# Performance work log

Measured on AMD Instinct MI355X. Metric: run time of the kernel, lower is better.

Reference implementation:

```python
import jax, jax.numpy as jnp
import numpy as np

REG_MAX = 16
NUM_CLASSES = 80
STRIDES = (8, 16, 32)
FEAT_SIZES = ((80, 80), (40, 40), (20, 20))
CLS_DIM = 256
REG_DIM = 256
B = 16


def setup_inputs() -> dict:
    key = jax.random.key(0)
    ks = jax.random.split(key, 32)
    inp = {}
    i = 0
    for l, (H, W) in enumerate(FEAT_SIZES):
        inp[f"cls_feat{l}"] = jax.random.normal(ks[i], (B, CLS_DIM, H, W), jnp.float32); i += 1
        inp[f"reg_feat{l}"] = jax.random.normal(ks[i], (B, REG_DIM, H, W), jnp.float32); i += 1
    bias_init = -float(np.log((1.0 - 0.01) / 0.01))
    for l in range(3):
        inp[f"obj_w{l}"] = jax.random.normal(ks[i], (1, REG_DIM), jnp.float32) * 0.02; i += 1
        inp[f"obj_b{l}"] = jnp.full((1,), bias_init, jnp.float32)
        inp[f"cls_w{l}"] = jax.random.normal(ks[i], (NUM_CLASSES, CLS_DIM), jnp.float32) * 0.02; i += 1
        inp[f"cls_b{l}"] = jnp.full((NUM_CLASSES,), bias_init, jnp.float32)
        inp[f"reg_w{l}"] = jax.random.normal(ks[i], (4 * REG_MAX, REG_DIM), jnp.float32) * 0.02; i += 1
        inp[f"reg_b{l}"] = jnp.ones((4 * REG_MAX,), jnp.float32)
    return inp


def _anchors(H, W, stride):
    ay, ax = jnp.meshgrid(jnp.arange(H, dtype=jnp.float32), jnp.arange(W, dtype=jnp.float32), indexing="ij")
    a = jnp.stack([ax, ay], axis=-1).reshape(-1, 2)  # [HW, 2] (x, y)
    return (a + 0.5) * stride


def _level(cls_feat, reg_feat, obj_w, obj_b, cls_w, cls_b, reg_w, reg_b, stride):
    Bb, _, H, W = cls_feat.shape
    M = H * W
    # 1x1 convs as channel contractions; output in [B, H, W, O] then flatten to [B, M, O]
    obj = (jnp.einsum("bchw,oc->bhwo", reg_feat, obj_w) + obj_b).reshape(Bb, M, 1)
    cls = (jnp.einsum("bchw,oc->bhwo", cls_feat, cls_w) + cls_b).reshape(Bb, M, NUM_CLASSES)
    reg = (jnp.einsum("bchw,oc->bhwo", reg_feat, reg_w) + reg_b).reshape(Bb, M, 4 * REG_MAX)
    # DFL decode: softmax over bins, expectation with proj = linspace(0, reg_max, reg_max)
    proj = jnp.linspace(0.0, float(REG_MAX), REG_MAX)
    dist = jax.nn.softmax(reg.reshape(Bb, M, 4, REG_MAX), axis=-1)
    reg_d = jnp.einsum("bmfr,r->bmf", dist, proj)  # [B, M, 4] (l, t, r, b)
    anchors = _anchors(H, W, stride)  # [M, 2]
    x1y1 = anchors[None] - reg_d[..., :2] * stride
    x2y2 = anchors[None] + reg_d[..., 2:] * stride
    box = jnp.concatenate([x1y1, x2y2], axis=-1)  # [B, M, 4]
    return jnp.concatenate([obj, cls, reg, box], axis=-1)  # [B, M, 1+80+64+4]


def reference(cls_feat0, cls_feat1, cls_feat2, reg_feat0, reg_feat1, reg_feat2,
              obj_w0, obj_b0, cls_w0, cls_b0, reg_w0, reg_b0,
              obj_w1, obj_b1, cls_w1, cls_b1, reg_w1, reg_b1,
              obj_w2, obj_b2, cls_w2, cls_b2, reg_w2, reg_b2):
    lvl0 = _level(cls_feat0, reg_feat0, obj_w0, obj_b0, cls_w0, cls_b0, reg_w0, reg_b0, STRIDES[0])
    lvl1 = _level(cls_feat1, reg_feat1, obj_w1, obj_b1, cls_w1, cls_b1, reg_w1, reg_b1, STRIDES[1])
    lvl2 = _level(cls_feat2, reg_feat2, obj_w2, obj_b2, cls_w2, cls_b2, reg_w2, reg_b2, STRIDES[2])
    # concat anchors along M: [B, 8400, 149]
    return jnp.concatenate([lvl0, lvl1, lvl2], axis=1)
```

## Files before the change

kernel.cpp:

```cpp
#include <hip/hip_runtime.h>
#include <stdint.h>

typedef __attribute__((ext_vector_type(4))) float f32x4;
typedef __attribute__((ext_vector_type(8))) short s16x8;

struct Params {
  const float* cls_feat[3];
  const float* reg_feat[3];
  const float* obj_w[3];
  const float* obj_b[3];
  const float* cls_w[3];
  const float* cls_b[3];
  const float* reg_w[3];
  const float* reg_b[3];
  float* out;
};

__device__ __forceinline__ unsigned short f2bf(float f) {
  unsigned int u = __builtin_bit_cast(unsigned int, f);
  u = (u + 0x7FFFu + ((u >> 16) & 1u)) >> 16;
  return (unsigned short)u;
}

#define LDS_PITCH 264

__global__ __launch_bounds__(320) void head_kernel(Params p) {
  const int tid  = threadIdx.x;
  const int lane = tid & 63;
  const int wave = tid >> 6;
  const int quad = lane >> 4;
  const int col  = lane & 15;
  const bool is_cls = (blockIdx.y == 0);

  int bx = blockIdx.x;
  int b  = bx / 132;
  int t  = bx - b * 132;
  int level, tloc;
  if (t < 100)      { level = 0; tloc = t; }
  else if (t < 125) { level = 1; tloc = t - 100; }
  else              { level = 2; tloc = t - 125; }

  const int   LW_[3]   = {80, 40, 20};
  const int   LM_[3]   = {6400, 1600, 400};
  const float LS_[3]   = {8.f, 16.f, 32.f};
  const int   LOFF_[3] = {0, 6400, 8000};

  const int   Mlvl = LM_[level];
  const int   Moff = LOFF_[level];
  const float strd = LS_[level];
  const int   m0   = tloc * 64;
  int valid = Mlvl - m0; if (valid > 64) valid = 64;

  __shared__ __align__(16) short lds_feat[64 * LDS_PITCH];
  __shared__ float g_lds[4][64];

  const float* featp = (is_cls ? p.cls_feat[level] : p.reg_feat[level])
                       + (size_t)b * 256 * (size_t)Mlvl;
  {
    const int mloc = tid & 63;
    int mg = m0 + mloc; if (mg > Mlvl - 1) mg = Mlvl - 1;
    const float* colp = featp + mg;
    for (int cb = wave; cb < 32; cb += 5) {
      const int c0 = cb * 8;
      float f[8];
      #pragma unroll
      for (int j = 0; j < 8; ++j) f[j] = colp[(size_t)(c0 + j) * Mlvl];
      s16x8 h;
      #pragma unroll
      for (int j = 0; j < 8; ++j) h[j] = (short)f2bf(f[j]);
      *(s16x8*)&lds_feat[mloc * LDS_PITCH + c0] = h;
    }
  }

  s16x8 afrag[8];
  {
    const int orow = wave * 16 + col;
    const float* wptr = nullptr;
    if (is_cls) {
      wptr = p.cls_w[level] + orow * 256;
    } else {
      if (orow < 64)       wptr = p.reg_w[level] + orow * 256;
      else if (orow == 64) wptr = p.obj_w[level];
    }
    #pragma unroll
    for (int s = 0; s < 8; ++s) {
      s16x8 a = {0, 0, 0, 0, 0, 0, 0, 0};
      if (wptr) {
        const f32x4* wp = (const f32x4*)(wptr + s * 32 + quad * 8);
        f32x4 w0 = wp[0], w1 = wp[1];
        a[0] = (short)f2bf(w0[0]); a[1] = (short)f2bf(w0[1]);
        a[2] = (short)f2bf(w0[2]); a[3] = (short)f2bf(w0[3]);
        a[4] = (short)f2bf(w1[0]); a[5] = (short)f2bf(w1[1]);
        a[6] = (short)f2bf(w1[2]); a[7] = (short)f2bf(w1[3]);
      }
      afrag[s] = a;
    }
  }

  float bias[4];
  #pragma unroll
  for (int r = 0; r < 4; ++r) {
    const int o = wave * 16 + quad * 4 + r;
    if (is_cls) bias[r] = p.cls_b[level][o];
    else        bias[r] = (o < 64) ? p.reg_b[level][o]
                        : ((o == 64) ? p.obj_b[level][0] : 0.f);
  }

  __syncthreads();

  f32x4 acc[4];
  #pragma unroll
  for (int mf = 0; mf < 4; ++mf) {
    f32x4 d = {0.f, 0.f, 0.f, 0.f};
    const short* brow = &lds_feat[(mf * 16 + col) * LDS_PITCH + quad * 8];
    #pragma unroll
    for (int s = 0; s < 8; ++s) {
      s16x8 bfrag = *(const s16x8*)(brow + s * 32);
      d = __builtin_amdgcn_mfma_f32_16x16x32_bf16(afrag[s], bfrag, d, 0, 0, 0);
    }
    acc[mf] = d;
  }

  const size_t outbase = (size_t)b * 8400 + Moff + m0;
  float* out = p.out;

  if (is_cls) {
    #pragma unroll
    for (int mf = 0; mf < 4; ++mf) {
      const int m = mf * 16 + col;
      if (m < valid) {
        const size_t rowp = (outbase + m) * 149 + 1 + wave * 16 + quad * 4;
        #pragma unroll
        for (int r = 0; r < 4; ++r) out[rowp + r] = acc[mf][r] + bias[r];
      }
    }
  } else if (wave < 4) {
    const float projscale = 16.f / 15.f;
    #pragma unroll
    for (int mf = 0; mf < 4; ++mf) {
      const int m = mf * 16 + col;
      const float v0 = acc[mf][0] + bias[0];
      const float v1 = acc[mf][1] + bias[1];
      const float v2 = acc[mf][2] + bias[2];
      const float v3 = acc[mf][3] + bias[3];
      if (m < valid) {
        const size_t rowp = (outbase + m) * 149 + 81 + wave * 16 + quad * 4;
        out[rowp + 0] = v0; out[rowp + 1] = v1;
        out[rowp + 2] = v2; out[rowp + 3] = v3;
      }
      float mx = fmaxf(fmaxf(v0, v1), fmaxf(v2, v3));
      mx = fmaxf(mx, __shfl_xor(mx, 16, 64));
      mx = fmaxf(mx, __shfl_xor(mx, 32, 64));
      const float e0 = __expf(v0 - mx), e1 = __expf(v1 - mx);
      const float e2 = __expf(v2 - mx), e3 = __expf(v3 - mx);
      float s = e0 + e1 + e2 + e3;
      const float q4 = (float)(quad * 4);
      float n = q4 * e0 + (q4 + 1.f) * e1 + (q4 + 2.f) * e2 + (q4 + 3.f) * e3;
      s += __shfl_xor(s, 16, 64); s += __shfl_xor(s, 32, 64);
      n += __shfl_xor(n, 16, 64); n += __shfl_xor(n, 32, 64);
      if (quad == 0) g_lds[wave][m] = projscale * n / s;
    }
  } else {
    #pragma unroll
    for (int mf = 0; mf < 4; ++mf) {
      const int m = mf * 16 + col;
      if (quad == 0 && m < valid)
        out[(outbase + m) * 149] = acc[mf][0] + bias[0];
    }
  }

  __syncthreads();

  if (!is_cls && wave == 4) {
    const int m = lane;
    if (m < valid) {
      const float g0 = g_lds[0][m], g1 = g_lds[1][m];
      const float g2 = g_lds[2][m], g3 = g_lds[3][m];
      const int mg = m0 + m;
      int hh;
      if (level == 0)      hh = mg / 80;
      else if (level == 1) hh = mg / 40;
      else                 hh = mg / 20;
      const int ww = mg - hh * LW_[level];
      const float ax = (ww + 0.5f) * strd;
      const float ay = (hh + 0.5f) * strd;
      const size_t rowp = (outbase + m) * 149 + 145;
      out[rowp + 0] = ax - g0 * strd;
      out[rowp + 1] = ay - g1 * strd;
      out[rowp + 2] = ax + g2 * strd;
      out[rowp + 3] = ay + g3 * strd;
    }
  }
}

extern "C" void kernel_launch(void* const* d_in, const int* in_sizes, int n_in,
                              void* d_out, int out_size, void* d_ws, size_t ws_size,
                              hipStream_t stream) {
  (void)in_sizes; (void)n_in; (void)out_size; (void)d_ws; (void)ws_size;
  Params p;
  p.cls_feat[0] = (const float*)d_in[0];
  p.reg_feat[0] = (const float*)d_in[1];
  p.cls_feat[1] = (const float*)d_in[2];
  p.reg_feat[1] = (const float*)d_in[3];
  p.cls_feat[2] = (const float*)d_in[4];
  p.reg_feat[2] = (const float*)d_in[5];
  for (int l = 0; l < 3; ++l) {
    const int base = 6 + l * 6;
    p.obj_w[l] = (const float*)d_in[base + 0];
    p.obj_b[l] = (const float*)d_in[base + 1];
    p.cls_w[l] = (const float*)d_in[base + 2];
    p.cls_b[l] = (const float*)d_in[base + 3];
    p.reg_w[l] = (const float*)d_in[base + 4];
    p.reg_b[l] = (const float*)d_in[base + 5];
  }
  p.out = (float*)d_out;

  dim3 grid(16 * 132, 2);
  dim3 block(320);
  hipLaunchKernelGGL(head_kernel, grid, block, 0, stream, p);
}
```

Measured before the change: 376.4 us.

## Use 80-anchor tiles with swizzled LDS, prefetched feature loads, vector stores

Tiles now cover 80 anchors instead of 64. Every level divides evenly, so the ragged tail checks go away and the grid shrinks. The padded LDS pitch is replaced by an XOR swizzle to avoid bank conflicts. Feature loads are double-buffered in registers so global reads overlap the bf16 conversion and LDS stores. Weight loads are issued before the conversions, and outputs are written with 16-byte memcpy stores. The cls path returns early and the box scratch reuses the feature LDS. The memcpy stores land on unaligned addresses because the output row stride is 149 floats, which may split into smaller stores.

```diff
diff --git a/kernel.cpp b/kernel.cpp
--- a/kernel.cpp
+++ b/kernel.cpp
@@ -22,9 +22,7 @@
   return (unsigned short)u;
 }
 
-#define LDS_PITCH 264
-
-__global__ __launch_bounds__(320) void head_kernel(Params p) {
+__global__ __launch_bounds__(320, 5) void head_kernel(Params p) {
   const int tid  = threadIdx.x;
   const int lane = tid & 63;
   const int wave = tid >> 6;
@@ -33,12 +31,12 @@
   const bool is_cls = (blockIdx.y == 0);
 
   int bx = blockIdx.x;
-  int b  = bx / 132;
-  int t  = bx - b * 132;
+  int b  = bx / 105;
+  int t  = bx - b * 105;
   int level, tloc;
-  if (t < 100)      { level = 0; tloc = t; }
-  else if (t < 125) { level = 1; tloc = t - 100; }
-  else              { level = 2; tloc = t - 125; }
+  if (t < 80)       { level = 0; tloc = t; }
+  else if (t < 100) { level = 1; tloc = t - 80; }
+  else              { level = 2; tloc = t - 100; }
 
   const int   LW_[3]   = {80, 40, 20};
   const int   LM_[3]   = {6400, 1600, 400};
@@ -48,77 +46,92 @@
   const int   Mlvl = LM_[level];
   const int   Moff = LOFF_[level];
   const float strd = LS_[level];
-  const int   m0   = tloc * 64;
-  int valid = Mlvl - m0; if (valid > 64) valid = 64;
-
-  __shared__ __align__(16) short lds_feat[64 * LDS_PITCH];
-  __shared__ float g_lds[4][64];
-
+  const int   m0   = tloc * 80;
+
+  __shared__ __align__(16) short lds_feat[80 * 256];
+
+  const f32x4 vzero = {0.f, 0.f, 0.f, 0.f};
+
+  const int orow = wave * 16 + col;
+  const float* wptr;
+  if (is_cls)          wptr = p.cls_w[level] + orow * 256;
+  else if (orow < 64)  wptr = p.reg_w[level] + orow * 256;
+  else if (orow == 64) wptr = p.obj_w[level];
+  else                 wptr = nullptr;
+
+  f32x4 wv[16];
+  #pragma unroll
+  for (int s = 0; s < 8; ++s) {
+    if (wptr) {
+      const f32x4* wp = (const f32x4*)(wptr + s * 32 + quad * 8);
+      wv[2 * s]     = wp[0];
+      wv[2 * s + 1] = wp[1];
+    } else {
+      wv[2 * s]     = vzero;
+      wv[2 * s + 1] = vzero;
+    }
+  }
+
+  f32x4 bias = vzero;
+  {
+    const int o0 = wave * 16 + quad * 4;
+    if (is_cls)        bias = *(const f32x4*)(p.cls_b[level] + o0);
+    else if (o0 < 64)  bias = *(const f32x4*)(p.reg_b[level] + o0);
+    else if (o0 == 64) bias[0] = p.obj_b[level][0];
+  }
+
+  const int mloc = tid % 80;
+  const int cb0  = tid / 80;
   const float* featp = (is_cls ? p.cls_feat[level] : p.reg_feat[level])
-                       + (size_t)b * 256 * (size_t)Mlvl;
-  {
-    const int mloc = tid & 63;
-    int mg = m0 + mloc; if (mg > Mlvl - 1) mg = Mlvl - 1;
-    const float* colp = featp + mg;
-    for (int cb = wave; cb < 32; cb += 5) {
-      const int c0 = cb * 8;
-      float f[8];
+                       + (size_t)b * 256 * (size_t)Mlvl + m0 + mloc;
+
+  float f[2][8];
+  #pragma unroll
+  for (int j = 0; j < 8; ++j) f[0][j] = featp[(size_t)(cb0 * 8 + j) * Mlvl];
+
+  s16x8 afrag[8];
+  #pragma unroll
+  for (int s = 0; s < 8; ++s) {
+    s16x8 a;
+    #pragma unroll
+    for (int j = 0; j < 4; ++j) {
+      a[j]     = (short)f2bf(wv[2 * s][j]);
+      a[4 + j] = (short)f2bf(wv[2 * s + 1][j]);
+    }
+    afrag[s] = a;
+  }
+
+  const int swz = mloc & 7;
+  #pragma unroll
+  for (int i = 0; i < 8; ++i) {
+    if (i < 7) {
+      const int cbn = cb0 + 4 * (i + 1);
       #pragma unroll
-      for (int j = 0; j < 8; ++j) f[j] = colp[(size_t)(c0 + j) * Mlvl];
-      s16x8 h;
-      #pragma unroll
-      for (int j = 0; j < 8; ++j) h[j] = (short)f2bf(f[j]);
-      *(s16x8*)&lds_feat[mloc * LDS_PITCH + c0] = h;
-    }
-  }
-
-  s16x8 afrag[8];
-  {
-    const int orow = wave * 16 + col;
-    const float* wptr = nullptr;
-    if (is_cls) {
-      wptr = p.cls_w[level] + orow * 256;
-    } else {
-      if (orow < 64)       wptr = p.reg_w[level] + orow * 256;
-      else if (orow == 64) wptr = p.obj_w[level];
-    }
+      for (int j = 0; j < 8; ++j)
+        f[(i + 1) & 1][j] = featp[(size_t)(cbn * 8 + j) * Mlvl];
+    }
+    const int cb = cb0 + 4 * i;
+    s16x8 h;
+    #pragma unroll
+    for (int j = 0; j < 8; ++j) h[j] = (short)f2bf(f[i & 1][j]);
+    *(s16x8*)&lds_feat[mloc * 256 + ((cb ^ swz) << 3)] = h;
+  }
+
+  __syncthreads();
+
+  f32x4 acc[5];
+  #pragma unroll
+  for (int mf = 0; mf < 5; ++mf) acc[mf] = vzero;
+  #pragma unroll
+  for (int mf = 0; mf < 5; ++mf) {
+    const int row = mf * 16 + col;
+    const short* base = &lds_feat[row * 256];
+    const int rswz = row & 7;
     #pragma unroll
     for (int s = 0; s < 8; ++s) {
-      s16x8 a = {0, 0, 0, 0, 0, 0, 0, 0};
-      if (wptr) {
-        const f32x4* wp = (const f32x4*)(wptr + s * 32 + quad * 8);
-        f32x4 w0 = wp[0], w1 = wp[1];
-        a[0] = (short)f2bf(w0[0]); a[1] = (short)f2bf(w0[1]);
-        a[2] = (short)f2bf(w0[2]); a[3] = (short)f2bf(w0[3]);
-        a[4] = (short)f2bf(w1[0]); a[5] = (short)f2bf(w1[1]);
-        a[6] = (short)f2bf(w1[2]); a[7] = (short)f2bf(w1[3]);
-      }
-      afrag[s] = a;
-    }
-  }
-
-  float bias[4];
-  #pragma unroll
-  for (int r = 0; r < 4; ++r) {
-    const int o = wave * 16 + quad * 4 + r;
-    if (is_cls) bias[r] = p.cls_b[level][o];
-    else        bias[r] = (o < 64) ? p.reg_b[level][o]
-                        : ((o == 64) ? p.obj_b[level][0] : 0.f);
-  }
-
-  __syncthreads();
-
-  f32x4 acc[4];
-  #pragma unroll
-  for (int mf = 0; mf < 4; ++mf) {
-    f32x4 d = {0.f, 0.f, 0.f, 0.f};
-    const short* brow = &lds_feat[(mf * 16 + col) * LDS_PITCH + quad * 8];
-    #pragma unroll
-    for (int s = 0; s < 8; ++s) {
-      s16x8 bfrag = *(const s16x8*)(brow + s * 32);
-      d = __builtin_amdgcn_mfma_f32_16x16x32_bf16(afrag[s], bfrag, d, 0, 0, 0);
-    }
-    acc[mf] = d;
+      s16x8 bfrag = *(const s16x8*)(base + (((s * 4 + quad) ^ rswz) << 3));
+      acc[mf] = __builtin_amdgcn_mfma_f32_16x16x32_bf16(afrag[s], bfrag, acc[mf], 0, 0, 0);
+    }
   }
 
   const size_t outbase = (size_t)b * 8400 + Moff + m0;
@@ -126,69 +139,69 @@
 
   if (is_cls) {
     #pragma unroll
-    for (int mf = 0; mf < 4; ++mf) {
+    for (int mf = 0; mf < 5; ++mf) {
       const int m = mf * 16 + col;
-      if (m < valid) {
-        const size_t rowp = (outbase + m) * 149 + 1 + wave * 16 + quad * 4;
-        #pragma unroll
-        for (int r = 0; r < 4; ++r) out[rowp + r] = acc[mf][r] + bias[r];
-      }
-    }
-  } else if (wave < 4) {
+      f32x4 v = acc[mf] + bias;
+      float* dst = out + (outbase + m) * 149 + 1 + wave * 16 + quad * 4;
+      __builtin_memcpy(dst, &v, 16);
+    }
+    return;
+  }
+
+  float* g_lds = (float*)lds_feat;
+  __syncthreads();
+
+  if (wave < 4) {
     const float projscale = 16.f / 15.f;
     #pragma unroll
-    for (int mf = 0; mf < 4; ++mf) {
+    for (int mf = 0; mf < 5; ++mf) {
       const int m = mf * 16 + col;
-      const float v0 = acc[mf][0] + bias[0];
-      const float v1 = acc[mf][1] + bias[1];
-      const float v2 = acc[mf][2] + bias[2];
-      const float v3 = acc[mf][3] + bias[3];
-      if (m < valid) {
-        const size_t rowp = (outbase + m) * 149 + 81 + wave * 16 + quad * 4;
-        out[rowp + 0] = v0; out[rowp + 1] = v1;
-        out[rowp + 2] = v2; out[rowp + 3] = v3;
-      }
-      float mx = fmaxf(fmaxf(v0, v1), fmaxf(v2, v3));
+      f32x4 v = acc[mf] + bias;
+      float* dst = out + (outbase + m) * 149 + 81 + wave * 16 + quad * 4;
+      __builtin_memcpy(dst, &v, 16);
+      float mx = fmaxf(fmaxf(v[0], v[1]), fmaxf(v[2], v[3]));
       mx = fmaxf(mx, __shfl_xor(mx, 16, 64));
       mx = fmaxf(mx, __shfl_xor(mx, 32, 64));
-      const float e0 = __expf(v0 - mx), e1 = __expf(v1 - mx);
-      const float e2 = __expf(v2 - mx), e3 = __expf(v3 - mx);
-      float s = e0 + e1 + e2 + e3;
+      const float e0 = __expf(v[0] - mx), e1 = __expf(v[1] - mx);
+      const float e2 = __expf(v[2] - mx), e3 = __expf(v[3] - mx);
+      float sden = e0 + e1 + e2 + e3;
       const float q4 = (float)(quad * 4);
       float n = q4 * e0 + (q4 + 1.f) * e1 + (q4 + 2.f) * e2 + (q4 + 3.f) * e3;
-      s += __shfl_xor(s, 16, 64); s += __shfl_xor(s, 32, 64);
-      n += __shfl_xor(n, 16, 64); n += __shfl_xor(n, 32, 64);
-      if (quad == 0) g_lds[wave][m] = projscale * n / s;
+      sden += __shfl_xor(sden, 16, 64); sden += __shfl_xor(sden, 32, 64);
+      n    += __shfl_xor(n, 16, 64);    n    += __shfl_xor(n, 32, 64);
+      if (quad == 0) g_lds[wave * 80 + m] = projscale * n / sden;
     }
   } else {
     #pragma unroll
-    for (int mf = 0; mf < 4; ++mf) {
+    for (int mf = 0; mf < 5; ++mf) {
       const int m = mf * 16 + col;
-      if (quad == 0 && m < valid)
-        out[(outbase + m) * 149] = acc[mf][0] + bias[0];
+      if (quad == 0) out[(outbase + m) * 149] = acc[mf][0] + bias[0];
     }
   }
 
   __syncthreads();
 
-  if (!is_cls && wave == 4) {
-    const int m = lane;
-    if (m < valid) {
-      const float g0 = g_lds[0][m], g1 = g_lds[1][m];
-      const float g2 = g_lds[2][m], g3 = g_lds[3][m];
-      const int mg = m0 + m;
-      int hh;
-      if (level == 0)      hh = mg / 80;
-      else if (level == 1) hh = mg / 40;
-      else                 hh = mg / 20;
-      const int ww = mg - hh * LW_[level];
-      const float ax = (ww + 0.5f) * strd;
-      const float ay = (hh + 0.5f) * strd;
-      const size_t rowp = (outbase + m) * 149 + 145;
-      out[rowp + 0] = ax - g0 * strd;
-      out[rowp + 1] = ay - g1 * strd;
-      out[rowp + 2] = ax + g2 * strd;
-      out[rowp + 3] = ay + g3 * strd;
+  if (wave == 4) {
+    #pragma unroll
+    for (int it = 0; it < 2; ++it) {
+      const int m = it * 64 + lane;
+      if (m < 80) {
+        const float g0 = g_lds[m], g1 = g_lds[80 + m];
+        const float g2 = g_lds[160 + m], g3 = g_lds[240 + m];
+        const int mg = m0 + m;
+        int hh;
+        if (level == 0)      hh = mg / 80;
+        else if (level == 1) hh = mg / 40;
+        else                 hh = mg / 20;
+        const int ww = mg - hh * LW_[level];
+        const float ax = (ww + 0.5f) * strd;
+        const float ay = (hh + 0.5f) * strd;
+        f32x4 bv;
+        bv[0] = ax - g0 * strd; bv[1] = ay - g1 * strd;
+        bv[2] = ax + g2 * strd; bv[3] = ay + g3 * strd;
+        float* dst = out + (outbase + m) * 149 + 145;
+        __builtin_memcpy(dst, &bv, 16);
+      }
     }
   }
 }
@@ -215,7 +228,7 @@
   }
   p.out = (float*)d_out;
 
-  dim3 grid(16 * 132, 2);
+  dim3 grid(16 * 105, 2);
   dim3 block(320);
   hipLaunchKernelGGL(head_kernel, grid, block, 0, stream, p);
 }
```

Result: faster. 358.7 us (-4.7%).
